# Kernel tuning notes

Measured on AMD Instinct MI355X. Metric: run time of the kernel, lower is better.

The kernel has to match this reference:

```python
import jax, jax.numpy as jnp
import numpy as np

LN_EPS = 1e-6  # flax.linen.LayerNorm default
ETA_BASE = 1.0  # TTTLinear default


def _ln(u, g, b):
    mu = u.mean(-1, keepdims=True)
    var = ((u - mu) ** 2).mean(-1, keepdims=True)
    return (u - mu) / jnp.sqrt(var + LN_EPS) * g + b


def setup_inputs() -> dict:
    key = jax.random.key(0)
    ks = jax.random.split(key, 8)
    B, T, D, Bd = 16, 2048, 512, 64
    s_in = 1.0 / np.sqrt(D)
    s_bn = 1.0 / np.sqrt(Bd)
    return {
        "x": jax.random.normal(ks[0], (B, T, D), jnp.float32),
        "Wk": jax.random.normal(ks[1], (D, Bd), jnp.float32) * s_in,
        "bk": jnp.zeros((Bd,), jnp.float32),
        "Wv": jax.random.normal(ks[2], (D, Bd), jnp.float32) * s_in,
        "bv": jnp.zeros((Bd,), jnp.float32),
        "Wq": jax.random.normal(ks[3], (D, Bd), jnp.float32) * s_in,
        "bq": jnp.zeros((Bd,), jnp.float32),
        "Wo": jax.random.normal(ks[4], (Bd, D), jnp.float32) * s_bn,
        "bo": jnp.zeros((D,), jnp.float32),
        "ln_g": jnp.ones((Bd,), jnp.float32),
        "ln_b": jnp.zeros((Bd,), jnp.float32),
        "lr_w": jax.random.normal(ks[5], (D,), jnp.float32) * s_in,
        "lr_b": jnp.zeros((), jnp.float32),
        "W0": jax.random.normal(ks[6], (Bd, Bd), jnp.float32) * 0.01,
    }


def reference(x, Wk, bk, Wv, bv, Wq, bq, Wo, bo, ln_g, ln_b, lr_w, lr_b, W0):
    # Sequential TTT-Linear: per-token SGD update of fast weights W (per batch element).
    B, T, D = x.shape
    Bd = W0.shape[0]

    def ssl_loss(W, k, v):
        # f(k; W) = k + LN(k @ W.T); loss = mean((f - v)^2)
        pred = k + _ln(k @ W.T, ln_g, ln_b)
        return jnp.mean((pred - v) ** 2)

    grad_fn = jax.vmap(jax.value_and_grad(ssl_loss))  # over batch

    def step(W, x_t):
        # x_t: (B, D); W: (B, Bd, Bd)
        k = x_t @ Wk + bk
        v = x_t @ Wv + bv
        loss, gW = grad_fn(W, k, v)
        eta = ETA_BASE * jax.nn.sigmoid(x_t @ lr_w + lr_b)  # (B,)
        W_new = W - eta[:, None, None] * gW
        q = x_t @ Wq + bq
        h = q + _ln(jnp.einsum('bi,boi->bo', q, W_new), ln_g, ln_b)
        z = h @ Wo + bo
        return W_new, (z, loss)

    W_init = jnp.broadcast_to(W0, (B, Bd, Bd))
    W_final, (zs, losses) = jax.lax.scan(step, W_init, jnp.swapaxes(x, 0, 1))
    z = jnp.swapaxes(zs, 0, 1)  # (B, T, D_out)
    return z
```

## Files before the change

kernel.cpp:

```cpp
#include <hip/hip_runtime.h>
#include <math.h>

#define NB 16
#define T  2048
#define D  512
#define BD 64
#define BT (NB*T)

#define OFF_K   0
#define OFF_V   (BT*BD)
#define OFF_Q   (2*BT*BD)
#define OFF_ETA (3*BT*BD)
#define OFF_H   (3*BT*BD + BT)

#define GSTRIDE 544
#define NCHUNK  (BT/16)

__device__ __forceinline__ float wave_allsum(float x) {
  x += __int_as_float(__builtin_amdgcn_update_dpp(
      0, __float_as_int(x), 0x111, 0xf, 0xf, true));
  x += __int_as_float(__builtin_amdgcn_update_dpp(
      0, __float_as_int(x), 0x112, 0xf, 0xf, true));
  x += __int_as_float(__builtin_amdgcn_update_dpp(
      0, __float_as_int(x), 0x114, 0xf, 0xf, true));
  x += __int_as_float(__builtin_amdgcn_update_dpp(
      0, __float_as_int(x), 0x118, 0xf, 0xf, true));
  x += __int_as_float(__builtin_amdgcn_update_dpp(
      0, __float_as_int(x), 0x142, 0xa, 0xf, false));
  x += __int_as_float(__builtin_amdgcn_update_dpp(
      0, __float_as_int(x), 0x143, 0xc, 0xf, false));
  return __int_as_float(__builtin_amdgcn_readlane(__float_as_int(x), 63));
}

__device__ __forceinline__ void lds_barrier() {
  __builtin_amdgcn_sched_barrier(0);
  __builtin_amdgcn_s_waitcnt(0xC07F);
  __builtin_amdgcn_s_barrier();
  __builtin_amdgcn_sched_barrier(0);
}

__device__ __forceinline__ void do_proj(const float* __restrict__ W,
                                        const float* __restrict__ bias,
                                        float* __restrict__ Out,
                                        const float* xs, int col, int rg,
                                        size_t row0) {
  float a0 = 0.f, a1 = 0.f, a2 = 0.f, a3 = 0.f;
  for (int d = 0; d < D; d += 4) {
    float w0 = W[(d + 0) * BD + col];
    float w1 = W[(d + 1) * BD + col];
    float w2 = W[(d + 2) * BD + col];
    float w3 = W[(d + 3) * BD + col];
    const float* xb = xs + (rg * 4) * D + d;
    float4 x0 = *(const float4*)(xb);
    float4 x1 = *(const float4*)(xb + D);
    float4 x2 = *(const float4*)(xb + 2 * D);
    float4 x3 = *(const float4*)(xb + 3 * D);
    a0 += x0.x * w0 + x0.y * w1 + x0.z * w2 + x0.w * w3;
    a1 += x1.x * w0 + x1.y * w1 + x1.z * w2 + x1.w * w3;
    a2 += x2.x * w0 + x2.y * w1 + x2.z * w2 + x2.w * w3;
    a3 += x3.x * w0 + x3.y * w1 + x3.z * w2 + x3.w * w3;
  }
  float bb = bias[col];
  Out[(row0 + rg * 4 + 0) * BD + col] = a0 + bb;
  Out[(row0 + rg * 4 + 1) * BD + col] = a1 + bb;
  Out[(row0 + rg * 4 + 2) * BD + col] = a2 + bb;
  Out[(row0 + rg * 4 + 3) * BD + col] = a3 + bb;
}

__global__ __launch_bounds__(256) void proj_kernel(
    const float* __restrict__ x,
    const float* __restrict__ Wk, const float* __restrict__ bk,
    const float* __restrict__ Wv, const float* __restrict__ bv,
    const float* __restrict__ Wq, const float* __restrict__ bq,
    float* __restrict__ Kout, float* __restrict__ Vout,
    float* __restrict__ Qout) {
  __shared__ __align__(16) float xs[16 * D];
  const int tid = threadIdx.x;
  const size_t row0 = (size_t)blockIdx.x * 16;
  const float4* xg = (const float4*)(x + row0 * D);
  float4* xs4 = (float4*)xs;
#pragma unroll
  for (int i = 0; i < 8; i++) xs4[i * 256 + tid] = xg[i * 256 + tid];
  __syncthreads();
  const int col = tid & 63;
  const int rg = tid >> 6;
  do_proj(Wk, bk, Kout, xs, col, rg, row0);
  do_proj(Wv, bv, Vout, xs, col, rg, row0);
  do_proj(Wq, bq, Qout, xs, col, rg, row0);
}

__global__ __launch_bounds__(256) void eta_kernel(const float* __restrict__ x,
                                                  const float* __restrict__ lr_w,
                                                  const float* __restrict__ lr_b,
                                                  float* __restrict__ eta) {
  const int tid = threadIdx.x;
  const int lane = tid & 63;
  const int wv = tid >> 6;
  const size_t r = (size_t)blockIdx.x * 4 + wv;
  const float* xr = x + r * D + lane * 8;
  float4 a = *(const float4*)xr;
  float4 b = *(const float4*)(xr + 4);
  const float* lw = lr_w + lane * 8;
  float4 la = *(const float4*)lw;
  float4 lb = *(const float4*)(lw + 4);
  float p = a.x * la.x + a.y * la.y + a.z * la.z + a.w * la.w +
            b.x * lb.x + b.y * lb.y + b.z * lb.z + b.w * lb.w;
#pragma unroll
  for (int m = 32; m > 0; m >>= 1) p += __shfl_xor(p, m, 64);
  if (lane == 0) eta[r] = 1.0f / (1.0f + expf(-(p + lr_b[0])));
}

__global__ __launch_bounds__(256) void gram_kernel(
    const float* __restrict__ K, const float* __restrict__ V,
    const float* __restrict__ Q, const float* __restrict__ ln_g,
    const float* __restrict__ ln_b, float* __restrict__ G) {
  __shared__ __align__(16) float sK[16][64], sQ[16][64], sV[16][64];
  __shared__ float sg[64], sb[64];
  const int tid = threadIdx.x;
  const size_t row0 = (size_t)blockIdx.x * 16;
  ((float4*)sK)[tid] = ((const float4*)(K + row0 * BD))[tid];
  ((float4*)sQ)[tid] = ((const float4*)(Q + row0 * BD))[tid];
  ((float4*)sV)[tid] = ((const float4*)(V + row0 * BD))[tid];
  if (tid < 64) { sg[tid] = ln_g[tid]; sb[tid] = ln_b[tid]; }
  __syncthreads();
  const int i = tid >> 4, t = tid & 15;
  float kk = 0.f, kq = 0.f;
#pragma unroll
  for (int d = 0; d < 64; d += 4) {
    float4 a4 = *(const float4*)&sK[i][d];
    float4 b4 = *(const float4*)&sK[t][d];
    float4 c4 = *(const float4*)&sQ[t][d];
    kk += a4.x * b4.x + a4.y * b4.y + a4.z * b4.z + a4.w * b4.w;
    kq += a4.x * c4.x + a4.y * c4.y + a4.z * c4.z + a4.w * c4.w;
  }
  size_t gb = (size_t)blockIdx.x * GSTRIDE;
  G[gb + i * 16 + t] = kk;
  G[gb + 256 + i * 16 + t] = kq;
  if (tid < 16) {
    float sc = 0.f;
    for (int d = 0; d < 64; d++)
      sc += sg[d] * (sK[tid][d] + sb[d] - sV[tid][d]);
    G[gb + 512 + tid] = sc;
  }
}

__global__ __launch_bounds__(256, 1)
void ttt_seq_kernel(
    const float* __restrict__ Kin, const float* __restrict__ Vin,
    const float* __restrict__ Qin, const float* __restrict__ eta_in,
    const float* __restrict__ W0, const float* __restrict__ ln_g,
    const float* __restrict__ ln_b, float* __restrict__ Hout,
    const float* __restrict__ gram) {
  __shared__ __align__(16) float2 part2[16][4][64];
  __shared__ __align__(16) float kls[16][64];
  __shared__ __align__(16) float qls[16][64];
  const int tid = threadIdx.x;
  const int lane = tid & 63;
  const int wvu = __builtin_amdgcn_readfirstlane(tid) >> 6;
  const int b = blockIdx.x;

  float w[16];
  {
    const float4* w04 = (const float4*)(W0 + (size_t)lane * BD + wvu * 16);
#pragma unroll
    for (int i = 0; i < 4; i++) {
      float4 t4 = w04[i];
      w[4 * i] = t4.x; w[4 * i + 1] = t4.y; w[4 * i + 2] = t4.z; w[4 * i + 3] = t4.w;
    }
  }
  const float g = ln_g[lane];
  const float bet = ln_b[lane];
  const float a = g * g;
  const float A2 = wave_allsum(a);

  size_t base = (size_t)b * T * BD;
  size_t ebase = (size_t)b * T;

  float krow[16], qrow[16], vrow[16];
#pragma unroll
  for (int r = 0; r < 16; r++) {
    krow[r] = Kin[base + r * BD + lane];
    qrow[r] = Qin[base + r * BD + lane];
    vrow[r] = Vin[base + r * BD + lane];
  }
  float ev  = eta_in[ebase + lane];
  float evn = eta_in[ebase + 64 + lane];

  float u2sv[4], qsv[4];

  for (int c64 = 0; c64 < 32; c64++) {
    size_t eoff = (size_t)(c64 + 2) * 64;
    if (eoff >= T) eoff = 0;
    float ev2 = eta_in[ebase + eoff + lane];

    for (int cc = 0; cc < 4; cc++) {
      const size_t gb = (size_t)(b * 128 + c64 * 4 + cc) * GSTRIDE;
      float KKr[15], KQr[16];
#pragma unroll
      for (int t = 0; t < 15; t++) KKr[t] = gram[gb + t * 16 + lane];
#pragma unroll
      for (int t = 0; t < 16; t++) KQr[t] = gram[gb + 256 + t * 16 + lane];
      float SCv = gram[gb + 512 + lane];

#pragma unroll
      for (int r = 0; r < 16; r++) {
        kls[r][lane] = krow[r];
        qls[r][lane] = qrow[r];
      }
      float4 kuf[3][4], quf[3][4];
#pragma unroll
      for (int r = 0; r < 3; r++) {
        const float4* kp = (const float4*)&kls[r][wvu * 16];
        const float4* qp = (const float4*)&qls[r][wvu * 16];
#pragma unroll
        for (int i = 0; i < 4; i++) { kuf[r][i] = kp[i]; quf[r][i] = qp[i]; }
      }
      float u0[16], p0[16];
#pragma unroll
      for (int r = 0; r < 16; r++) {
        const int bf = r % 3;
        float uu0 = 0.f, uu1 = 0.f, uu2 = 0.f, uu3 = 0.f;
        float pp0 = 0.f, pp1 = 0.f, pp2 = 0.f, pp3 = 0.f;
#pragma unroll
        for (int i = 0; i < 4; i++) {
          uu0 += kuf[bf][i].x * w[4 * i + 0];
          uu1 += kuf[bf][i].y * w[4 * i + 1];
          uu2 += kuf[bf][i].z * w[4 * i + 2];
          uu3 += kuf[bf][i].w * w[4 * i + 3];
          pp0 += quf[bf][i].x * w[4 * i + 0];
          pp1 += quf[bf][i].y * w[4 * i + 1];
          pp2 += quf[bf][i].z * w[4 * i + 2];
          pp3 += quf[bf][i].w * w[4 * i + 3];
        }
        part2[r][wvu][lane] = make_float2((uu0 + uu1) + (uu2 + uu3),
                                          (pp0 + pp1) + (pp2 + pp3));
        if (r < 13) {
          const float4* kp = (const float4*)&kls[r + 3][wvu * 16];
          const float4* qp = (const float4*)&qls[r + 3][wvu * 16];
#pragma unroll
          for (int i = 0; i < 4; i++) { kuf[bf][i] = kp[i]; quf[bf][i] = qp[i]; }
        }
      }

      lds_barrier();

#pragma unroll
      for (int r = 0; r < 16; r++) {
        float2 pA = part2[r][0][lane];
        float2 pB = part2[r][1][lane];
        float2 pC = part2[r][2][lane];
        float2 pD = part2[r][3][lane];
        u0[r] = (pA.x + pB.x) + (pC.x + pD.x);
        p0[r] = (pA.y + pB.y) + (pC.y + pD.y);
      }

#pragma unroll
      for (int t = 0; t < 16; t++) {
        float u = u0[t];
        float kcur = krow[t], vcur = vrow[t], qcur = qrow[t];
        float ecur = __int_as_float(
            __builtin_amdgcn_readlane(__float_as_int(ev), cc * 16 + t));
        float c0 = g * (kcur + bet - vcur);

        float Su   = wave_allsum(u);
        float Suu  = wave_allsum(u * u);
        float Sau  = wave_allsum(a * u);
        float Sauu = wave_allsum(a * u * u);
        float Scu  = wave_allsum(c0 * u);
        float Sc   = __int_as_float(
            __builtin_amdgcn_readlane(__float_as_int(SCv), t));

        float mu = Su * (1.0f / 64);
        float var = Suu * (1.0f / 64) - mu * mu;
        float rstd = rsqrtf(var + 1e-6f);
        float xh = (u - mu) * rstd;
        float Axh   = rstd * (Sau - mu * A2);
        float Scxh  = rstd * (Scu - mu * Sc);
        float Saxh2 = rstd * rstd * (Sauu - 2.0f * mu * Sau + mu * mu * A2);
        float s1 = (2.0f / 64) * (Sc + Axh);
        float s2 = (2.0f / 64) * (Scxh + Saxh2);
        float dxh = (2.0f / 64) * (c0 + a * xh);
        float dldu = rstd * (dxh - s1 * (1.0f / 64) - xh * (s2 * (1.0f / 64)));
        float coef = -ecur * dldu;

        if (t < 15)
          u0[t + 1] += coef * __int_as_float(
              __builtin_amdgcn_readlane(__float_as_int(KKr[t]), t + 1));
#pragma unroll
        for (int s = t + 2; s < 16; s++)
          u0[s] += coef * __int_as_float(
              __builtin_amdgcn_readlane(__float_as_int(KKr[t]), s));
#pragma unroll
        for (int s = t; s < 16; s++)
          p0[s] += coef * __int_as_float(
              __builtin_amdgcn_readlane(__float_as_int(KQr[t]), s));

        {
          const float4* kp = (const float4*)&kls[t][wvu * 16];
#pragma unroll
          for (int i = 0; i < 4; i++) {
            float4 k4 = kp[i];
            w[4 * i + 0] += coef * k4.x;
            w[4 * i + 1] += coef * k4.y;
            w[4 * i + 2] += coef * k4.z;
            w[4 * i + 3] += coef * k4.w;
          }
        }

        if ((t & 3) == wvu) { u2sv[t >> 2] = p0[t]; qsv[t >> 2] = qcur; }

        krow[t] = Kin[base + 16 * BD + lane];
        qrow[t] = Qin[base + 16 * BD + lane];
        vrow[t] = Vin[base + 16 * BD + lane];
        base += BD;
      }

#pragma unroll
      for (int fi = 0; fi < 4; fi++) {
        float u2 = u2sv[fi];
        float Su2  = wave_allsum(u2);
        float Suu2 = wave_allsum(u2 * u2);
        float mu2 = Su2 * (1.0f / 64);
        float rstd2 = rsqrtf(Suu2 * (1.0f / 64) - mu2 * mu2 + 1e-6f);
        int tt = 4 * fi + wvu;
        Hout[base - (size_t)(16 - tt) * BD + lane] =
            qsv[fi] + (u2 - mu2) * rstd2 * g + bet;
      }

      lds_barrier();
    }
    ev = evn; evn = ev2;
  }
}

__global__ __launch_bounds__(256) void outproj_kernel(
    const float* __restrict__ H, const float* __restrict__ Wo,
    const float* __restrict__ bo, float* __restrict__ out) {
  __shared__ __align__(16) float ht[16 * BD];
  const int tid = threadIdx.x;
  const size_t row0 = (size_t)blockIdx.x * 16;
  ((float4*)ht)[tid] = ((const float4*)(H + row0 * BD))[tid];
  __syncthreads();
  float acc0[16], acc1[16];
#pragma unroll
  for (int r = 0; r < 16; r++) { acc0[r] = 0.f; acc1[r] = 0.f; }
  for (int kk = 0; kk < BD; kk++) {
    float w0 = Wo[kk * D + tid];
    float w1 = Wo[kk * D + tid + 256];
#pragma unroll
    for (int r = 0; r < 16; r++) {
      float hv = ht[r * BD + kk];
      acc0[r] += hv * w0;
      acc1[r] += hv * w1;
    }
  }
  float b0 = bo[tid], b1 = bo[tid + 256];
#pragma unroll
  for (int r = 0; r < 16; r++) {
    out[(row0 + r) * D + tid] = acc0[r] + b0;
    out[(row0 + r) * D + tid + 256] = acc1[r] + b1;
  }
}

extern "C" void kernel_launch(void* const* d_in, const int* in_sizes, int n_in,
                              void* d_out, int out_size, void* d_ws,
                              size_t ws_size, hipStream_t stream) {
  (void)in_sizes; (void)n_in; (void)out_size; (void)ws_size;
  const float* x    = (const float*)d_in[0];
  const float* Wk   = (const float*)d_in[1];
  const float* bk   = (const float*)d_in[2];
  const float* Wv   = (const float*)d_in[3];
  const float* bv   = (const float*)d_in[4];
  const float* Wq   = (const float*)d_in[5];
  const float* bq   = (const float*)d_in[6];
  const float* Wo   = (const float*)d_in[7];
  const float* bo   = (const float*)d_in[8];
  const float* ln_g = (const float*)d_in[9];
  const float* ln_b = (const float*)d_in[10];
  const float* lr_w = (const float*)d_in[11];
  const float* lr_b = (const float*)d_in[12];
  const float* W0   = (const float*)d_in[13];

  float* ws  = (float*)d_ws;
  float* Kb  = ws + OFF_K;
  float* Vb  = ws + OFF_V;
  float* Qb  = ws + OFF_Q;
  float* ETA = ws + OFF_ETA;
  float* Hb  = ws + OFF_H;
  float* out = (float*)d_out;
  float* GRAM = out;

  proj_kernel<<<BT / 16, 256, 0, stream>>>(x, Wk, bk, Wv, bv, Wq, bq, Kb, Vb, Qb);
  eta_kernel<<<BT / 4, 256, 0, stream>>>(x, lr_w, lr_b, ETA);
  gram_kernel<<<NCHUNK, 256, 0, stream>>>(Kb, Vb, Qb, ln_g, ln_b, GRAM);
  ttt_seq_kernel<<<NB, 256, 0, stream>>>(Kb, Vb, Qb, ETA, W0, ln_g, ln_b, Hb, GRAM);
  outproj_kernel<<<BT / 16, 256, 0, stream>>>(Hb, Wo, bo, out);
}
```

Measured before the change: 1.436 ms.

## Split sequential TTT kernel across 8 waves and defer query-correction terms

The sequential per-batch kernel now runs with 512 threads (8 waves), so each wave owns 8 columns of the fast weight instead of 16, halving the per-wave rank-1 update and matvec work. The partial sums are reduced through an extra LDS stage split across waves. The per-token incremental update of the query projections (p0) is removed from the serial loop. Instead each wave reconstructs its two output rows afterwards from saved coefficients and a column of the KQ gram, shortening the critical path. It adds an extra barrier and the redundant per-wave serial LN-gradient work still runs on all 8 waves.

Result: slower. 1.923 ms (+33.9%).

```diff
diff --git a/kernel.cpp b/kernel.cpp
--- a/kernel.cpp
+++ b/kernel.cpp
@@ -144,14 +144,15 @@
   }
 }
 
-__global__ __launch_bounds__(256, 1)
+__global__ __launch_bounds__(512, 2)
 void ttt_seq_kernel(
     const float* __restrict__ Kin, const float* __restrict__ Vin,
     const float* __restrict__ Qin, const float* __restrict__ eta_in,
     const float* __restrict__ W0, const float* __restrict__ ln_g,
     const float* __restrict__ ln_b, float* __restrict__ Hout,
     const float* __restrict__ gram) {
-  __shared__ __align__(16) float2 part2[16][4][64];
+  __shared__ __align__(16) float2 part2[16][8][64];
+  __shared__ __align__(16) float2 fin[16][64];
   __shared__ __align__(16) float kls[16][64];
   __shared__ __align__(16) float qls[16][64];
   const int tid = threadIdx.x;
@@ -159,14 +160,12 @@
   const int wvu = __builtin_amdgcn_readfirstlane(tid) >> 6;
   const int b = blockIdx.x;
 
-  float w[16];
+  float w[8];
   {
-    const float4* w04 = (const float4*)(W0 + (size_t)lane * BD + wvu * 16);
-#pragma unroll
-    for (int i = 0; i < 4; i++) {
-      float4 t4 = w04[i];
-      w[4 * i] = t4.x; w[4 * i + 1] = t4.y; w[4 * i + 2] = t4.z; w[4 * i + 3] = t4.w;
-    }
+    const float4* w04 = (const float4*)(W0 + (size_t)lane * BD + wvu * 8);
+    float4 t0 = w04[0], t1 = w04[1];
+    w[0] = t0.x; w[1] = t0.y; w[2] = t0.z; w[3] = t0.w;
+    w[4] = t1.x; w[5] = t1.y; w[6] = t1.z; w[7] = t1.w;
   }
   const float g = ln_g[lane];
   const float bet = ln_b[lane];
@@ -186,73 +185,73 @@
   float ev  = eta_in[ebase + lane];
   float evn = eta_in[ebase + 64 + lane];
 
-  float u2sv[4], qsv[4];
-
   for (int c64 = 0; c64 < 32; c64++) {
     size_t eoff = (size_t)(c64 + 2) * 64;
     if (eoff >= T) eoff = 0;
     float ev2 = eta_in[ebase + eoff + lane];
 
     for (int cc = 0; cc < 4; cc++) {
-      const size_t gb = (size_t)(b * 128 + c64 * 4 + cc) * GSTRIDE;
-      float KKr[15], KQr[16];
+      const int n = c64 * 4 + cc;
+      const size_t gb = (size_t)(b * 128 + n) * GSTRIDE;
+      float KKr[15];
 #pragma unroll
       for (int t = 0; t < 15; t++) KKr[t] = gram[gb + t * 16 + lane];
-#pragma unroll
-      for (int t = 0; t < 16; t++) KQr[t] = gram[gb + 256 + t * 16 + lane];
       float SCv = gram[gb + 512 + lane];
+      float KQcA = gram[gb + 256 + (size_t)lane * 16 + wvu];
+      float KQcB = gram[gb + 256 + (size_t)lane * 16 + wvu + 8];
 
 #pragma unroll
       for (int r = 0; r < 16; r++) {
         kls[r][lane] = krow[r];
         qls[r][lane] = qrow[r];
       }
-      float4 kuf[3][4], quf[3][4];
-#pragma unroll
-      for (int r = 0; r < 3; r++) {
-        const float4* kp = (const float4*)&kls[r][wvu * 16];
-        const float4* qp = (const float4*)&qls[r][wvu * 16];
-#pragma unroll
-        for (int i = 0; i < 4; i++) { kuf[r][i] = kp[i]; quf[r][i] = qp[i]; }
-      }
+#pragma unroll
+      for (int r = 0; r < 16; r++) {
+        const float4* kp = (const float4*)&kls[r][wvu * 8];
+        const float4* qp = (const float4*)&qls[r][wvu * 8];
+        float4 k0 = kp[0], k1 = kp[1], q0 = qp[0], q1 = qp[1];
+        float ua = k0.x * w[0] + k0.y * w[1] + k0.z * w[2] + k0.w * w[3];
+        float ub = k1.x * w[4] + k1.y * w[5] + k1.z * w[6] + k1.w * w[7];
+        float pa = q0.x * w[0] + q0.y * w[1] + q0.z * w[2] + q0.w * w[3];
+        float pb = q1.x * w[4] + q1.y * w[5] + q1.z * w[6] + q1.w * w[7];
+        part2[r][wvu][lane] = make_float2(ua + ub, pa + pb);
+      }
+
+      lds_barrier();
+
+      {
+        const int r0 = wvu * 2;
+#pragma unroll
+        for (int rr = 0; rr < 2; rr++) {
+          const int r = r0 + rr;
+          float2 s0 = part2[r][0][lane];
+          float2 s1 = part2[r][1][lane];
+          float2 s2 = part2[r][2][lane];
+          float2 s3 = part2[r][3][lane];
+          float2 s4 = part2[r][4][lane];
+          float2 s5 = part2[r][5][lane];
+          float2 s6 = part2[r][6][lane];
+          float2 s7 = part2[r][7][lane];
+          float su = ((s0.x + s1.x) + (s2.x + s3.x)) +
+                     ((s4.x + s5.x) + (s6.x + s7.x));
+          float sp = ((s0.y + s1.y) + (s2.y + s3.y)) +
+                     ((s4.y + s5.y) + (s6.y + s7.y));
+          fin[r][lane] = make_float2(su, sp);
+        }
+      }
+
+      lds_barrier();
+
       float u0[16], p0[16];
 #pragma unroll
       for (int r = 0; r < 16; r++) {
-        const int bf = r % 3;
-        float uu0 = 0.f, uu1 = 0.f, uu2 = 0.f, uu3 = 0.f;
-        float pp0 = 0.f, pp1 = 0.f, pp2 = 0.f, pp3 = 0.f;
-#pragma unroll
-        for (int i = 0; i < 4; i++) {
-          uu0 += kuf[bf][i].x * w[4 * i + 0];
-          uu1 += kuf[bf][i].y * w[4 * i + 1];
-          uu2 += kuf[bf][i].z * w[4 * i + 2];
-          uu3 += kuf[bf][i].w * w[4 * i + 3];
-          pp0 += quf[bf][i].x * w[4 * i + 0];
-          pp1 += quf[bf][i].y * w[4 * i + 1];
-          pp2 += quf[bf][i].z * w[4 * i + 2];
-          pp3 += quf[bf][i].w * w[4 * i + 3];
-        }
-        part2[r][wvu][lane] = make_float2((uu0 + uu1) + (uu2 + uu3),
-                                          (pp0 + pp1) + (pp2 + pp3));
-        if (r < 13) {
-          const float4* kp = (const float4*)&kls[r + 3][wvu * 16];
-          const float4* qp = (const float4*)&qls[r + 3][wvu * 16];
-#pragma unroll
-          for (int i = 0; i < 4; i++) { kuf[bf][i] = kp[i]; quf[bf][i] = qp[i]; }
-        }
-      }
-
-      lds_barrier();
-
-#pragma unroll
-      for (int r = 0; r < 16; r++) {
-        float2 pA = part2[r][0][lane];
-        float2 pB = part2[r][1][lane];
-        float2 pC = part2[r][2][lane];
-        float2 pD = part2[r][3][lane];
-        u0[r] = (pA.x + pB.x) + (pC.x + pD.x);
-        p0[r] = (pA.y + pB.y) + (pC.y + pD.y);
-      }
+        float2 f2 = fin[r][lane];
+        u0[r] = f2.x;
+        p0[r] = f2.y;
+      }
+
+      float coefs[16];
+      float p0sv0 = 0.f, p0sv1 = 0.f, qsv0 = 0.f, qsv1 = 0.f;
 
 #pragma unroll
       for (int t = 0; t < 16; t++) {
@@ -282,6 +281,7 @@
         float dxh = (2.0f / 64) * (c0 + a * xh);
         float dldu = rstd * (dxh - s1 * (1.0f / 64) - xh * (s2 * (1.0f / 64)));
         float coef = -ecur * dldu;
+        coefs[t] = coef;
 
         if (t < 15)
           u0[t + 1] += coef * __int_as_float(
@@ -290,24 +290,20 @@
         for (int s = t + 2; s < 16; s++)
           u0[s] += coef * __int_as_float(
               __builtin_amdgcn_readlane(__float_as_int(KKr[t]), s));
-#pragma unroll
-        for (int s = t; s < 16; s++)
-          p0[s] += coef * __int_as_float(
-              __builtin_amdgcn_readlane(__float_as_int(KQr[t]), s));
+
+        if ((t & 7) == wvu) {
+          if (t < 8) { p0sv0 = p0[t]; qsv0 = qcur; }
+          else       { p0sv1 = p0[t]; qsv1 = qcur; }
+        }
 
         {
-          const float4* kp = (const float4*)&kls[t][wvu * 16];
-#pragma unroll
-          for (int i = 0; i < 4; i++) {
-            float4 k4 = kp[i];
-            w[4 * i + 0] += coef * k4.x;
-            w[4 * i + 1] += coef * k4.y;
-            w[4 * i + 2] += coef * k4.z;
-            w[4 * i + 3] += coef * k4.w;
-          }
+          const float4* kp = (const float4*)&kls[t][wvu * 8];
+          float4 k0 = kp[0], k1 = kp[1];
+          w[0] += coef * k0.x; w[1] += coef * k0.y;
+          w[2] += coef * k0.z; w[3] += coef * k0.w;
+          w[4] += coef * k1.x; w[5] += coef * k1.y;
+          w[6] += coef * k1.z; w[7] += coef * k1.w;
         }
-
-        if ((t & 3) == wvu) { u2sv[t >> 2] = p0[t]; qsv[t >> 2] = qcur; }
 
         krow[t] = Kin[base + 16 * BD + lane];
         qrow[t] = Qin[base + 16 * BD + lane];
@@ -315,16 +311,35 @@
         base += BD;
       }
 
-#pragma unroll
-      for (int fi = 0; fi < 4; fi++) {
-        float u2 = u2sv[fi];
+      {
+        float u2 = p0sv0;
+#pragma unroll
+        for (int i = 0; i < 8; i++) {
+          float term = coefs[i] * __int_as_float(
+              __builtin_amdgcn_readlane(__float_as_int(KQcA), i));
+          u2 += (i <= wvu) ? term : 0.f;
+        }
         float Su2  = wave_allsum(u2);
         float Suu2 = wave_allsum(u2 * u2);
         float mu2 = Su2 * (1.0f / 64);
         float rstd2 = rsqrtf(Suu2 * (1.0f / 64) - mu2 * mu2 + 1e-6f);
-        int tt = 4 * fi + wvu;
-        Hout[base - (size_t)(16 - tt) * BD + lane] =
-            qsv[fi] + (u2 - mu2) * rstd2 * g + bet;
+        Hout[base - (size_t)(16 - wvu) * BD + lane] =
+            qsv0 + (u2 - mu2) * rstd2 * g + bet;
+      }
+      {
+        float u2 = p0sv1;
+#pragma unroll
+        for (int i = 0; i < 16; i++) {
+          float term = coefs[i] * __int_as_float(
+              __builtin_amdgcn_readlane(__float_as_int(KQcB), i));
+          u2 += (i <= wvu + 8) ? term : 0.f;
+        }
+        float Su2  = wave_allsum(u2);
+        float Suu2 = wave_allsum(u2 * u2);
+        float mu2 = Su2 * (1.0f / 64);
+        float rstd2 = rsqrtf(Suu2 * (1.0f / 64) - mu2 * mu2 + 1e-6f);
+        Hout[base - (size_t)(8 - wvu) * BD + lane] =
+            qsv1 + (u2 - mu2) * rstd2 * g + bet;
       }
 
       lds_barrier();
@@ -393,6 +408,6 @@
   proj_kernel<<<BT / 16, 256, 0, stream>>>(x, Wk, bk, Wv, bv, Wq, bq, Kb, Vb, Qb);
   eta_kernel<<<BT / 4, 256, 0, stream>>>(x, lr_w, lr_b, ETA);
   gram_kernel<<<NCHUNK, 256, 0, stream>>>(Kb, Vb, Qb, ln_g, ln_b, GRAM);
-  ttt_seq_kernel<<<NB, 256, 0, stream>>>(Kb, Vb, Qb, ETA, W0, ln_g, ln_b, Hb, GRAM);
+  ttt_seq_kernel<<<NB, 512, 0, stream>>>(Kb, Vb, Qb, ETA, W0, ln_g, ln_b, Hb, GRAM);
   outproj_kernel<<<BT / 16, 256, 0, stream>>>(Hb, Wo, bo, out);
 }
```

## Split sequential TTT kernel into helper waves and a lagged critical-path wave

Applied to the files above, without the earlier changes.

The sequential kernel now runs five waves. Four helper waves compute the next chunk's W·k and W·q products into LDS with atomics, apply the weight updates one chunk late, and finish the output LayerNorm. A fifth wave runs only the serial per-token gradient recurrence, correcting the stale products with cross-chunk Gram terms (K_prev·K_cur and K_prev·Q_cur), which the gram kernel now also computes. The goal is to take the matmuls and weight updates off the serial critical path so they overlap with the recurrence. The cost is extra Gram work, a larger Gram buffer, more readlane work on the critical wave, and LDS atomics.

Result: slower. 2.276 ms (+58.4%).

```diff
diff --git a/kernel.cpp b/kernel.cpp
--- a/kernel.cpp
+++ b/kernel.cpp
@@ -13,9 +13,11 @@
 #define OFF_ETA (3*BT*BD)
 #define OFF_H   (3*BT*BD + BT)
 
-#define GSTRIDE 544
+#define GSTRIDE 1280
 #define NCHUNK  (BT/16)
 
+#define RL(x, i) __int_as_float(__builtin_amdgcn_readlane(__float_as_int(x), (i)))
+
 __device__ __forceinline__ float wave_allsum(float x) {
   x += __int_as_float(__builtin_amdgcn_update_dpp(
       0, __float_as_int(x), 0x111, 0xf, 0xf, true));
@@ -29,7 +31,7 @@
       0, __float_as_int(x), 0x142, 0xa, 0xf, false));
   x += __int_as_float(__builtin_amdgcn_update_dpp(
       0, __float_as_int(x), 0x143, 0xc, 0xf, false));
-  return __int_as_float(__builtin_amdgcn_readlane(__float_as_int(x), 63));
+  return RL(x, 63);
 }
 
 __device__ __forceinline__ void lds_barrier() {
@@ -115,27 +117,38 @@
     const float* __restrict__ Q, const float* __restrict__ ln_g,
     const float* __restrict__ ln_b, float* __restrict__ G) {
   __shared__ __align__(16) float sK[16][64], sQ[16][64], sV[16][64];
+  __shared__ __align__(16) float sK2[16][64], sQ2[16][64];
   __shared__ float sg[64], sb[64];
   const int tid = threadIdx.x;
   const size_t row0 = (size_t)blockIdx.x * 16;
-  ((float4*)sK)[tid] = ((const float4*)(K + row0 * BD))[tid];
-  ((float4*)sQ)[tid] = ((const float4*)(Q + row0 * BD))[tid];
-  ((float4*)sV)[tid] = ((const float4*)(V + row0 * BD))[tid];
+  const bool last = (blockIdx.x % 128) == 127;
+  const size_t row0n = last ? row0 : row0 + 16;
+  ((float4*)sK)[tid]  = ((const float4*)(K + row0 * BD))[tid];
+  ((float4*)sQ)[tid]  = ((const float4*)(Q + row0 * BD))[tid];
+  ((float4*)sV)[tid]  = ((const float4*)(V + row0 * BD))[tid];
+  ((float4*)sK2)[tid] = ((const float4*)(K + row0n * BD))[tid];
+  ((float4*)sQ2)[tid] = ((const float4*)(Q + row0n * BD))[tid];
   if (tid < 64) { sg[tid] = ln_g[tid]; sb[tid] = ln_b[tid]; }
   __syncthreads();
   const int i = tid >> 4, t = tid & 15;
-  float kk = 0.f, kq = 0.f;
+  float kk = 0.f, kq = 0.f, kkx = 0.f, kqx = 0.f;
 #pragma unroll
   for (int d = 0; d < 64; d += 4) {
     float4 a4 = *(const float4*)&sK[i][d];
     float4 b4 = *(const float4*)&sK[t][d];
     float4 c4 = *(const float4*)&sQ[t][d];
-    kk += a4.x * b4.x + a4.y * b4.y + a4.z * b4.z + a4.w * b4.w;
-    kq += a4.x * c4.x + a4.y * c4.y + a4.z * c4.z + a4.w * c4.w;
+    float4 d4 = *(const float4*)&sK2[t][d];
+    float4 e4 = *(const float4*)&sQ2[t][d];
+    kk  += a4.x * b4.x + a4.y * b4.y + a4.z * b4.z + a4.w * b4.w;
+    kq  += a4.x * c4.x + a4.y * c4.y + a4.z * c4.z + a4.w * c4.w;
+    kkx += a4.x * d4.x + a4.y * d4.y + a4.z * d4.z + a4.w * d4.w;
+    kqx += a4.x * e4.x + a4.y * e4.y + a4.z * e4.z + a4.w * e4.w;
   }
   size_t gb = (size_t)blockIdx.x * GSTRIDE;
   G[gb + i * 16 + t] = kk;
   G[gb + 256 + i * 16 + t] = kq;
+  G[gb + 768 + i * 16 + t] = kkx;
+  G[gb + 1024 + i * 16 + t] = kqx;
   if (tid < 16) {
     float sc = 0.f;
     for (int d = 0; d < 64; d++)
@@ -144,131 +157,210 @@
   }
 }
 
-__global__ __launch_bounds__(256, 1)
+__global__ __launch_bounds__(320, 1)
 void ttt_seq_kernel(
     const float* __restrict__ Kin, const float* __restrict__ Vin,
     const float* __restrict__ Qin, const float* __restrict__ eta_in,
     const float* __restrict__ W0, const float* __restrict__ ln_g,
     const float* __restrict__ ln_b, float* __restrict__ Hout,
     const float* __restrict__ gram) {
-  __shared__ __align__(16) float2 part2[16][4][64];
-  __shared__ __align__(16) float kls[16][64];
-  __shared__ __align__(16) float qls[16][64];
+  __shared__ __align__(16) float rK[4][16][64];
+  __shared__ __align__(16) float rQ[4][16][64];
+  __shared__ __align__(16) float rV[4][16][64];
+  __shared__ __align__(16) float fU[3][16][64];
+  __shared__ __align__(16) float fP[4][16][64];
+  __shared__ __align__(16) float cfl[3][16][64];
   const int tid = threadIdx.x;
   const int lane = tid & 63;
-  const int wvu = __builtin_amdgcn_readfirstlane(tid) >> 6;
+  const int wid = __builtin_amdgcn_readfirstlane(tid) >> 6;
+  const bool isHelper = wid < 4;
+  const int h = wid;
   const int b = blockIdx.x;
 
+  const float g = ln_g[lane];
+  const float bet = ln_b[lane];
+  const float a = g * g;
+
+  const size_t base = (size_t)b * T * BD;
+  const size_t ebase = (size_t)b * T;
+  const size_t gbase = (size_t)b * 128 * GSTRIDE;
+
   float w[16];
-  {
-    const float4* w04 = (const float4*)(W0 + (size_t)lane * BD + wvu * 16);
+  float A2 = 0.f;
+  if (isHelper) {
+    const float4* w04 = (const float4*)(W0 + (size_t)lane * BD + h * 16);
 #pragma unroll
     for (int i = 0; i < 4; i++) {
       float4 t4 = w04[i];
       w[4 * i] = t4.x; w[4 * i + 1] = t4.y; w[4 * i + 2] = t4.z; w[4 * i + 3] = t4.w;
     }
-  }
-  const float g = ln_g[lane];
-  const float bet = ln_b[lane];
-  const float a = g * g;
-  const float A2 = wave_allsum(a);
-
-  size_t base = (size_t)b * T * BD;
-  size_t ebase = (size_t)b * T;
-
-  float krow[16], qrow[16], vrow[16];
-#pragma unroll
-  for (int r = 0; r < 16; r++) {
-    krow[r] = Kin[base + r * BD + lane];
-    qrow[r] = Qin[base + r * BD + lane];
-    vrow[r] = Vin[base + r * BD + lane];
-  }
-  float ev  = eta_in[ebase + lane];
-  float evn = eta_in[ebase + 64 + lane];
-
-  float u2sv[4], qsv[4];
-
-  for (int c64 = 0; c64 < 32; c64++) {
-    size_t eoff = (size_t)(c64 + 2) * 64;
-    if (eoff >= T) eoff = 0;
-    float ev2 = eta_in[ebase + eoff + lane];
-
-    for (int cc = 0; cc < 4; cc++) {
-      const size_t gb = (size_t)(b * 128 + c64 * 4 + cc) * GSTRIDE;
-      float KKr[15], KQr[16];
-#pragma unroll
-      for (int t = 0; t < 15; t++) KKr[t] = gram[gb + t * 16 + lane];
-#pragma unroll
-      for (int t = 0; t < 16; t++) KQr[t] = gram[gb + 256 + t * 16 + lane];
+    ((float4*)rK[0])[tid] = ((const float4*)(Kin + base))[tid];
+    ((float4*)rQ[0])[tid] = ((const float4*)(Qin + base))[tid];
+    ((float4*)rV[0])[tid] = ((const float4*)(Vin + base))[tid];
+    ((float4*)rK[1])[tid] = ((const float4*)(Kin + base + 1024))[tid];
+    ((float4*)rQ[1])[tid] = ((const float4*)(Qin + base + 1024))[tid];
+    ((float4*)rV[1])[tid] = ((const float4*)(Vin + base + 1024))[tid];
+    float4 z4 = make_float4(0.f, 0.f, 0.f, 0.f);
+    ((float4*)fU[0])[tid] = z4; ((float4*)fU[1])[tid] = z4;
+    ((float4*)fP[0])[tid] = z4; ((float4*)fP[1])[tid] = z4;
+  } else {
+    A2 = wave_allsum(a);
+  }
+  lds_barrier();
+  if (isHelper) {
+#pragma unroll
+    for (int r = 0; r < 16; r++) {
+      const float4* kp = (const float4*)&rK[0][r][h * 16];
+      const float4* qp = (const float4*)&rQ[0][r][h * 16];
+      float4 k0 = kp[0], k1 = kp[1], k2 = kp[2], k3 = kp[3];
+      float4 q0 = qp[0], q1 = qp[1], q2 = qp[2], q3 = qp[3];
+      float u0s = k0.x*w[0]+k0.y*w[1]+k0.z*w[2]+k0.w*w[3];
+      float u1s = k1.x*w[4]+k1.y*w[5]+k1.z*w[6]+k1.w*w[7];
+      float u2s = k2.x*w[8]+k2.y*w[9]+k2.z*w[10]+k2.w*w[11];
+      float u3s = k3.x*w[12]+k3.y*w[13]+k3.z*w[14]+k3.w*w[15];
+      float p0s = q0.x*w[0]+q0.y*w[1]+q0.z*w[2]+q0.w*w[3];
+      float p1s = q1.x*w[4]+q1.y*w[5]+q1.z*w[6]+q1.w*w[7];
+      float p2s = q2.x*w[8]+q2.y*w[9]+q2.z*w[10]+q2.w*w[11];
+      float p3s = q3.x*w[12]+q3.y*w[13]+q3.z*w[14]+q3.w*w[15];
+      atomicAdd(&fU[0][r][lane], (u0s + u1s) + (u2s + u3s));
+      atomicAdd(&fP[0][r][lane], (p0s + p1s) + (p2s + p3s));
+    }
+  }
+  lds_barrier();
+
+  float coefs_prev[16], coefs_cur[16];
+#pragma unroll
+  for (int i = 0; i < 16; i++) coefs_prev[i] = 0.f;
+
+  for (int n = 0; n < 128; n++) {
+    const int rs = n & 3, rs1 = (n + 1) & 3, rs2 = (n + 2) & 3, rsm = (n - 1) & 3;
+    const int fu = n % 3, fu1 = (n + 1) % 3, fu2 = (n + 2) % 3;
+    const int fp1 = (n + 1) & 3, fpm = (n - 1) & 3, fp2 = (n + 2) & 3;
+
+    if (isHelper) {
+      float4 sk_ = ((const float4*)(Kin + base + (size_t)(n + 2) * 1024))[tid];
+      float4 sq_ = ((const float4*)(Qin + base + (size_t)(n + 2) * 1024))[tid];
+      float4 sv_ = ((const float4*)(Vin + base + (size_t)(n + 2) * 1024))[tid];
+
+      float cfH[16], cfHp[16];
+      if (n >= 1) {
+        const int s1 = (n - 1) % 3;
+#pragma unroll
+        for (int i = 0; i < 16; i++) cfH[i] = cfl[s1][i][lane];
+      } else {
+#pragma unroll
+        for (int i = 0; i < 16; i++) cfH[i] = 0.f;
+      }
+      if (n >= 2) {
+        const int s2 = (n - 2) % 3;
+#pragma unroll
+        for (int i = 0; i < 16; i++) cfHp[i] = cfl[s2][i][lane];
+      } else {
+#pragma unroll
+        for (int i = 0; i < 16; i++) cfHp[i] = 0.f;
+      }
+
+      if (n >= 1) {
+        const size_t gbm  = gbase + (size_t)(n - 1) * GSTRIDE;
+        const size_t gbm2 = gbase + (size_t)(n >= 2 ? n - 2 : 0) * GSTRIDE;
+        float KQc[4], KQXc[4];
+#pragma unroll
+        for (int j = 0; j < 4; j++) {
+          KQc[j]  = gram[gbm  + 256  + (size_t)lane * 16 + 4 * j + h];
+          KQXc[j] = gram[gbm2 + 1024 + (size_t)lane * 16 + 4 * j + h];
+        }
+#pragma unroll
+        for (int j = 0; j < 4; j++) {
+          const int s = 4 * j + h;
+          float u2 = fP[fpm][4 * j + h][lane];
+#pragma unroll
+          for (int i = 0; i < 16; i++) u2 += cfHp[i] * RL(KQXc[j], i);
+#pragma unroll
+          for (int i = 0; i < 16; i++) {
+            float term = cfH[i] * RL(KQc[j], i);
+            u2 += (i <= s) ? term : 0.f;
+          }
+          float Su2  = wave_allsum(u2);
+          float Suu2 = wave_allsum(u2 * u2);
+          float mu2 = Su2 * (1.0f / 64);
+          float rstd2 = rsqrtf(Suu2 * (1.0f / 64) - mu2 * mu2 + 1e-6f);
+          float qv = rQ[rsm][s][lane];
+          Hout[base + (size_t)((n - 1) * 16 + s) * BD + lane] =
+              qv + (u2 - mu2) * rstd2 * g + bet;
+        }
+#pragma unroll
+        for (int i = 0; i < 16; i++) {
+          const float4* kp = (const float4*)&rK[rsm][i][h * 16];
+          float4 k0 = kp[0], k1 = kp[1], k2 = kp[2], k3 = kp[3];
+          float cf = cfH[i];
+          w[0]  += cf * k0.x; w[1]  += cf * k0.y; w[2]  += cf * k0.z; w[3]  += cf * k0.w;
+          w[4]  += cf * k1.x; w[5]  += cf * k1.y; w[6]  += cf * k1.z; w[7]  += cf * k1.w;
+          w[8]  += cf * k2.x; w[9]  += cf * k2.y; w[10] += cf * k2.z; w[11] += cf * k2.w;
+          w[12] += cf * k3.x; w[13] += cf * k3.y; w[14] += cf * k3.z; w[15] += cf * k3.w;
+        }
+      }
+
+      if (n < 127) {
+#pragma unroll
+        for (int r = 0; r < 16; r++) {
+          const float4* kp = (const float4*)&rK[rs1][r][h * 16];
+          const float4* qp = (const float4*)&rQ[rs1][r][h * 16];
+          float4 k0 = kp[0], k1 = kp[1], k2 = kp[2], k3 = kp[3];
+          float4 q0 = qp[0], q1 = qp[1], q2 = qp[2], q3 = qp[3];
+          float u0s = k0.x*w[0]+k0.y*w[1]+k0.z*w[2]+k0.w*w[3];
+          float u1s = k1.x*w[4]+k1.y*w[5]+k1.z*w[6]+k1.w*w[7];
+          float u2s = k2.x*w[8]+k2.y*w[9]+k2.z*w[10]+k2.w*w[11];
+          float u3s = k3.x*w[12]+k3.y*w[13]+k3.z*w[14]+k3.w*w[15];
+          float p0s = q0.x*w[0]+q0.y*w[1]+q0.z*w[2]+q0.w*w[3];
+          float p1s = q1.x*w[4]+q1.y*w[5]+q1.z*w[6]+q1.w*w[7];
+          float p2s = q2.x*w[8]+q2.y*w[9]+q2.z*w[10]+q2.w*w[11];
+          float p3s = q3.x*w[12]+q3.y*w[13]+q3.z*w[14]+q3.w*w[15];
+          atomicAdd(&fU[fu1][r][lane], (u0s + u1s) + (u2s + u3s));
+          atomicAdd(&fP[fp1][r][lane], (p0s + p1s) + (p2s + p3s));
+        }
+      }
+
+      float4 z4 = make_float4(0.f, 0.f, 0.f, 0.f);
+      ((float4*)fU[fu2])[tid] = z4;
+      ((float4*)fP[fp2])[tid] = z4;
+      ((float4*)rK[rs2])[tid] = sk_;
+      ((float4*)rQ[rs2])[tid] = sq_;
+      ((float4*)rV[rs2])[tid] = sv_;
+    } else {
+      const size_t gb  = gbase + (size_t)n * GSTRIDE;
+      const size_t gbp = gbase + (size_t)(n >= 1 ? n - 1 : 0) * GSTRIDE;
+      float KKr[16];
+#pragma unroll
+      for (int t = 1; t < 16; t++) KKr[t] = gram[gb + t * 16 + lane];
+      float KKXc[16];
+#pragma unroll
+      for (int t = 0; t < 16; t++)
+        KKXc[t] = gram[gbp + 768 + (size_t)lane * 16 + t];
       float SCv = gram[gb + 512 + lane];
-
-#pragma unroll
-      for (int r = 0; r < 16; r++) {
-        kls[r][lane] = krow[r];
-        qls[r][lane] = qrow[r];
-      }
-      float4 kuf[3][4], quf[3][4];
-#pragma unroll
-      for (int r = 0; r < 3; r++) {
-        const float4* kp = (const float4*)&kls[r][wvu * 16];
-        const float4* qp = (const float4*)&qls[r][wvu * 16];
-#pragma unroll
-        for (int i = 0; i < 4; i++) { kuf[r][i] = kp[i]; quf[r][i] = qp[i]; }
-      }
-      float u0[16], p0[16];
-#pragma unroll
-      for (int r = 0; r < 16; r++) {
-        const int bf = r % 3;
-        float uu0 = 0.f, uu1 = 0.f, uu2 = 0.f, uu3 = 0.f;
-        float pp0 = 0.f, pp1 = 0.f, pp2 = 0.f, pp3 = 0.f;
-#pragma unroll
-        for (int i = 0; i < 4; i++) {
-          uu0 += kuf[bf][i].x * w[4 * i + 0];
-          uu1 += kuf[bf][i].y * w[4 * i + 1];
-          uu2 += kuf[bf][i].z * w[4 * i + 2];
-          uu3 += kuf[bf][i].w * w[4 * i + 3];
-          pp0 += quf[bf][i].x * w[4 * i + 0];
-          pp1 += quf[bf][i].y * w[4 * i + 1];
-          pp2 += quf[bf][i].z * w[4 * i + 2];
-          pp3 += quf[bf][i].w * w[4 * i + 3];
-        }
-        part2[r][wvu][lane] = make_float2((uu0 + uu1) + (uu2 + uu3),
-                                          (pp0 + pp1) + (pp2 + pp3));
-        if (r < 13) {
-          const float4* kp = (const float4*)&kls[r + 3][wvu * 16];
-          const float4* qp = (const float4*)&qls[r + 3][wvu * 16];
-#pragma unroll
-          for (int i = 0; i < 4; i++) { kuf[bf][i] = kp[i]; quf[bf][i] = qp[i]; }
-        }
-      }
-
-      lds_barrier();
-
-#pragma unroll
-      for (int r = 0; r < 16; r++) {
-        float2 pA = part2[r][0][lane];
-        float2 pB = part2[r][1][lane];
-        float2 pC = part2[r][2][lane];
-        float2 pD = part2[r][3][lane];
-        u0[r] = (pA.x + pB.x) + (pC.x + pD.x);
-        p0[r] = (pA.y + pB.y) + (pC.y + pD.y);
-      }
+      float ecv = eta_in[ebase + n * 16 + (lane & 15)];
+
+      float u0p[16];
+#pragma unroll
+      for (int t = 0; t < 16; t++) u0p[t] = fU[fu][t][lane];
 
 #pragma unroll
       for (int t = 0; t < 16; t++) {
-        float u = u0[t];
-        float kcur = krow[t], vcur = vrow[t], qcur = qrow[t];
-        float ecur = __int_as_float(
-            __builtin_amdgcn_readlane(__float_as_int(ev), cc * 16 + t));
-        float c0 = g * (kcur + bet - vcur);
+        float kc = rK[rs][t][lane];
+        float vc = rV[rs][t][lane];
+        float c0 = g * (kc + bet - vc);
+        float u = u0p[t];
+#pragma unroll
+        for (int i = 0; i < 16; i++) u += coefs_prev[i] * RL(KKXc[t], i);
+#pragma unroll
+        for (int i = 0; i < t; i++) u += coefs_cur[i] * RL(KKr[t], i);
 
         float Su   = wave_allsum(u);
         float Suu  = wave_allsum(u * u);
         float Sau  = wave_allsum(a * u);
         float Sauu = wave_allsum(a * u * u);
         float Scu  = wave_allsum(c0 * u);
-        float Sc   = __int_as_float(
-            __builtin_amdgcn_readlane(__float_as_int(SCv), t));
+        float Sc   = RL(SCv, t);
+        float ecur = RL(ecv, t);
 
         float mu = Su * (1.0f / 64);
         float var = Suu * (1.0f / 64) - mu * mu;
@@ -282,54 +374,46 @@
         float dxh = (2.0f / 64) * (c0 + a * xh);
         float dldu = rstd * (dxh - s1 * (1.0f / 64) - xh * (s2 * (1.0f / 64)));
         float coef = -ecur * dldu;
-
-        if (t < 15)
-          u0[t + 1] += coef * __int_as_float(
-              __builtin_amdgcn_readlane(__float_as_int(KKr[t]), t + 1));
-#pragma unroll
-        for (int s = t + 2; s < 16; s++)
-          u0[s] += coef * __int_as_float(
-              __builtin_amdgcn_readlane(__float_as_int(KKr[t]), s));
-#pragma unroll
-        for (int s = t; s < 16; s++)
-          p0[s] += coef * __int_as_float(
-              __builtin_amdgcn_readlane(__float_as_int(KQr[t]), s));
-
-        {
-          const float4* kp = (const float4*)&kls[t][wvu * 16];
-#pragma unroll
-          for (int i = 0; i < 4; i++) {
-            float4 k4 = kp[i];
-            w[4 * i + 0] += coef * k4.x;
-            w[4 * i + 1] += coef * k4.y;
-            w[4 * i + 2] += coef * k4.z;
-            w[4 * i + 3] += coef * k4.w;
-          }
-        }
-
-        if ((t & 3) == wvu) { u2sv[t >> 2] = p0[t]; qsv[t >> 2] = qcur; }
-
-        krow[t] = Kin[base + 16 * BD + lane];
-        qrow[t] = Qin[base + 16 * BD + lane];
-        vrow[t] = Vin[base + 16 * BD + lane];
-        base += BD;
-      }
-
-#pragma unroll
-      for (int fi = 0; fi < 4; fi++) {
-        float u2 = u2sv[fi];
-        float Su2  = wave_allsum(u2);
-        float Suu2 = wave_allsum(u2 * u2);
-        float mu2 = Su2 * (1.0f / 64);
-        float rstd2 = rsqrtf(Suu2 * (1.0f / 64) - mu2 * mu2 + 1e-6f);
-        int tt = 4 * fi + wvu;
-        Hout[base - (size_t)(16 - tt) * BD + lane] =
-            qsv[fi] + (u2 - mu2) * rstd2 * g + bet;
-      }
-
-      lds_barrier();
-    }
-    ev = evn; evn = ev2;
+        coefs_cur[t] = coef;
+        cfl[n % 3][t][lane] = coef;
+      }
+#pragma unroll
+      for (int i = 0; i < 16; i++) coefs_prev[i] = coefs_cur[i];
+    }
+    lds_barrier();
+  }
+
+  if (isHelper) {
+    float cfH[16], cfHp[16];
+#pragma unroll
+    for (int i = 0; i < 16; i++) { cfH[i] = cfl[127 % 3][i][lane]; cfHp[i] = cfl[126 % 3][i][lane]; }
+    const size_t gbm  = gbase + (size_t)127 * GSTRIDE;
+    const size_t gbm2 = gbase + (size_t)126 * GSTRIDE;
+    float KQc[4], KQXc[4];
+#pragma unroll
+    for (int j = 0; j < 4; j++) {
+      KQc[j]  = gram[gbm  + 256  + (size_t)lane * 16 + 4 * j + h];
+      KQXc[j] = gram[gbm2 + 1024 + (size_t)lane * 16 + 4 * j + h];
+    }
+#pragma unroll
+    for (int j = 0; j < 4; j++) {
+      const int s = 4 * j + h;
+      float u2 = fP[127 & 3][s][lane];
+#pragma unroll
+      for (int i = 0; i < 16; i++) u2 += cfHp[i] * RL(KQXc[j], i);
+#pragma unroll
+      for (int i = 0; i < 16; i++) {
+        float term = cfH[i] * RL(KQc[j], i);
+        u2 += (i <= s) ? term : 0.f;
+      }
+      float Su2  = wave_allsum(u2);
+      float Suu2 = wave_allsum(u2 * u2);
+      float mu2 = Su2 * (1.0f / 64);
+      float rstd2 = rsqrtf(Suu2 * (1.0f / 64) - mu2 * mu2 + 1e-6f);
+      float qv = rQ[127 & 3][s][lane];
+      Hout[base + (size_t)(127 * 16 + s) * BD + lane] =
+          qv + (u2 - mu2) * rstd2 * g + bet;
+    }
   }
 }
 
@@ -393,6 +477,6 @@
   proj_kernel<<<BT / 16, 256, 0, stream>>>(x, Wk, bk, Wv, bv, Wq, bq, Kb, Vb, Qb);
   eta_kernel<<<BT / 4, 256, 0, stream>>>(x, lr_w, lr_b, ETA);
   gram_kernel<<<NCHUNK, 256, 0, stream>>>(Kb, Vb, Qb, ln_g, ln_b, GRAM);
-  ttt_seq_kernel<<<NB, 256, 0, stream>>>(Kb, Vb, Qb, ETA, W0, ln_g, ln_b, Hb, GRAM);
+  ttt_seq_kernel<<<NB, 320, 0, stream>>>(Kb, Vb, Qb, ETA, W0, ln_g, ln_b, Hb, GRAM);
   outproj_kernel<<<BT / 16, 256, 0, stream>>>(Hb, Wo, bo, out);
 }
```
